# Kernel tuning notes

Hardware: AMD Instinct MI355X
Metric: run time of the kernel (lower is better)

Reference implementation:

```python
import jax, jax.numpy as jnp
import numpy as np

EMBED_DIM = 2048
NUM_HEADS = 16
HEAD_DIM = EMBED_DIM // NUM_HEADS  # 128
BLOCK_SIZE = 16
NUM_BLOCKS = 256  # max_seq_len 4096 / block_size 16
B = 64
T = 1  # single decode token per sequence (loop indexes k[i, 0, 0])


def setup_inputs() -> dict:
    key = jax.random.key(0)
    ks = jax.random.split(key, 12)
    w = 0.02
    return {
        "x": jax.random.normal(ks[0], (B, T, EMBED_DIM), jnp.float32),
        "k_cache": jax.random.normal(ks[1], (B, NUM_BLOCKS, BLOCK_SIZE, HEAD_DIM), jnp.float32),
        "v_cache": jax.random.normal(ks[2], (B, NUM_BLOCKS, BLOCK_SIZE, HEAD_DIM), jnp.float32),
        "cache_positions": jax.random.randint(ks[3], (B,), 0, NUM_BLOCKS * BLOCK_SIZE, jnp.int32),
        "Wq": jax.random.normal(ks[4], (EMBED_DIM, EMBED_DIM), jnp.float32) * w,
        "bq": jax.random.normal(ks[5], (EMBED_DIM,), jnp.float32) * w,
        "Wk": jax.random.normal(ks[6], (EMBED_DIM, HEAD_DIM), jnp.float32) * w,
        "bk": jax.random.normal(ks[7], (HEAD_DIM,), jnp.float32) * w,
        "Wv": jax.random.normal(ks[8], (EMBED_DIM, HEAD_DIM), jnp.float32) * w,
        "bv": jax.random.normal(ks[9], (HEAD_DIM,), jnp.float32) * w,
        "Wo": jax.random.normal(ks[10], (EMBED_DIM, EMBED_DIM), jnp.float32) * w,
        "bo": jax.random.normal(ks[11], (EMBED_DIM,), jnp.float32) * w,
    }


def reference(x, k_cache, v_cache, cache_positions, Wq, bq, Wk, bk, Wv, bv, Wo, bo):
    b, t, c = x.shape  # t == 1 (decode)
    hd = Wk.shape[1]
    h = c // hd
    scale = 1.0 / jnp.sqrt(jnp.asarray(hd, x.dtype))

    q = (x @ Wq + bq).reshape(b, t, h, hd)          # [B,1,H,hd]
    k_new = (x @ Wk + bk)[:, 0, :]                  # [B,hd] single KV head
    v_new = (x @ Wv + bv)[:, 0, :]                  # [B,hd]

    # Paged scatter: flatten (num_blocks, block_size) -> S slots; write new token at pos.
    s = k_cache.shape[1] * k_cache.shape[2]
    bidx = jnp.arange(b)
    kc = k_cache.reshape(b, s, hd).at[bidx, cache_positions].set(k_new)  # [B,S,hd]
    vc = v_cache.reshape(b, s, hd).at[bidx, cache_positions].set(v_new)

    # MQA: single KV head broadcast across H query heads. NOTE: softmax over the
    # FULL flattened cache (no validity mask), matching the original module.
    scores = jnp.einsum("bthd,bsd->bhts", q, kc) * scale   # [B,H,1,S]
    attn = jax.nn.softmax(scores, axis=-1)
    out = jnp.einsum("bhts,bsd->bthd", attn, vc).reshape(b, t, c)
    return out @ Wo + bo
```

## Files before the change

kernel.cpp:

```cpp
#include <hip/hip_runtime.h>
#include <math.h>

#define EMBED   2048
#define NHEADS  16
#define HD      128
#define S_TOT   4096
#define BATCH   64

typedef __attribute__((ext_vector_type(8))) short short8v;
typedef __attribute__((ext_vector_type(4))) short short4v;
typedef __attribute__((ext_vector_type(2))) short short2v;
typedef __attribute__((ext_vector_type(4))) float floatx4;

__device__ __forceinline__ unsigned short f2bf(float f) {
    unsigned u = __builtin_bit_cast(unsigned, f);
    u += 0x7fffu + ((u >> 16) & 1u);
    return (unsigned short)(u >> 16);
}

template <int CTRL>
__device__ __forceinline__ float dppf(float x) {
    int r = __builtin_amdgcn_mov_dpp(__builtin_bit_cast(int, x), CTRL, 0xF, 0xF, false);
    return __builtin_bit_cast(float, r);
}
__device__ __forceinline__ float rowmax16(float v) {
    v = fmaxf(v, dppf<0x121>(v));
    v = fmaxf(v, dppf<0x122>(v));
    v = fmaxf(v, dppf<0x124>(v));
    v = fmaxf(v, dppf<0x128>(v));
    return v;
}
__device__ __forceinline__ float rowsum16(float v) {
    v += dppf<0x121>(v);
    v += dppf<0x122>(v);
    v += dppf<0x124>(v);
    v += dppf<0x128>(v);
    return v;
}

__launch_bounds__(256)
__global__ void k1_qkv(const float* __restrict__ x,
                       const float* __restrict__ Wq, const float* __restrict__ bq,
                       const float* __restrict__ Wk, const float* __restrict__ bk,
                       const float* __restrict__ Wv, const float* __restrict__ bv,
                       float* __restrict__ qbuf, float* __restrict__ knew,
                       float* __restrict__ vnew) {
    const int tx = threadIdx.x & 31;
    const int ty = threadIdx.x >> 5;
    const int nt = blockIdx.x;
    const int kc = blockIdx.y;
    const int k0 = kc * 256;
    const int col0 = nt * 32;

    const float* W; const float* bias; float* out; int ldW;
    int cbase;
    if (col0 < 2048)       { W = Wq; bias = bq; out = qbuf; ldW = 2048; cbase = col0; }
    else if (col0 < 2176)  { W = Wk; bias = bk; out = knew; ldW = 128;  cbase = col0 - 2048; }
    else                   { W = Wv; bias = bv; out = vnew; ldW = 128;  cbase = col0 - 2176; }
    const int col = cbase + tx;

    __shared__ __align__(16) float xs[64][68];

    float acc[8] = {0, 0, 0, 0, 0, 0, 0, 0};

    for (int sub = 0; sub < 4; ++sub) {
        const int kb = k0 + sub * 64;
        #pragma unroll
        for (int i = 0; i < 4; ++i) {
            int c = threadIdx.x + i * 256;
            int r = c >> 4;
            int cc = (c & 15) << 2;
            float4 v = *(const float4*)(x + (size_t)r * EMBED + kb + cc);
            *(float4*)&xs[r][cc] = v;
        }
        __syncthreads();
        #pragma unroll
        for (int kk = 0; kk < 64; kk += 4) {
            float w0 = W[(size_t)(kb + kk + 0) * ldW + col];
            float w1 = W[(size_t)(kb + kk + 1) * ldW + col];
            float w2 = W[(size_t)(kb + kk + 2) * ldW + col];
            float w3 = W[(size_t)(kb + kk + 3) * ldW + col];
            #pragma unroll
            for (int j = 0; j < 8; ++j) {
                int m = ty + (j << 3);
                float4 xv = *(const float4*)&xs[m][kk];
                acc[j] = fmaf(xv.x, w0, acc[j]);
                acc[j] = fmaf(xv.y, w1, acc[j]);
                acc[j] = fmaf(xv.z, w2, acc[j]);
                acc[j] = fmaf(xv.w, w3, acc[j]);
            }
        }
        __syncthreads();
    }
    if (kc == 0) {
        float b = bias[col];
        #pragma unroll
        for (int j = 0; j < 8; ++j) acc[j] += b;
    }
    const int ldO = (ldW == 2048) ? 2048 : 128;
    #pragma unroll
    for (int j = 0; j < 8; ++j)
        atomicAdd(&out[(size_t)(ty + (j << 3)) * ldO + col], acc[j]);
}

__launch_bounds__(256)
__global__ void k2_attn(const float* __restrict__ qbuf,
                        const float* __restrict__ kcache,
                        const float* __restrict__ vcache,
                        const float* __restrict__ knew,
                        const float* __restrict__ vnew,
                        const int* __restrict__ cpos,
                        float* __restrict__ part_o,
                        float* __restrict__ part_ml)
{
    const int b = blockIdx.y;
    const int chunk = blockIdx.x;
    const int tid = threadIdx.x;
    const int w = tid >> 6;
    const int lane = tid & 63;
    const int quad = lane >> 4;
    const int lm = lane & 15;
    const int pos = cpos[b];

    __shared__ __align__(16) short qs[16 * 136];
    __shared__ __align__(16) short ksh[4][16 * 136];
    __shared__ __align__(16) short vsh[4][64 * 40];
    __shared__ __align__(16) short psh[4][16 * 40];

    {
        const int h = tid >> 4, d0 = (tid & 15) << 3;
        const float* src = qbuf + (size_t)b * EMBED + h * HD + d0;
        float4 a = *(const float4*)src;
        float4 c = *(const float4*)(src + 4);
        const float s = 0.08838834764831845f;
        short8v pk;
        pk[0] = f2bf(a.x * s); pk[1] = f2bf(a.y * s);
        pk[2] = f2bf(a.z * s); pk[3] = f2bf(a.w * s);
        pk[4] = f2bf(c.x * s); pk[5] = f2bf(c.y * s);
        pk[6] = f2bf(c.z * s); pk[7] = f2bf(c.w * s);
        *(short8v*)&qs[h * 136 + d0] = pk;
    }
    __syncthreads();

    short8v aq[4];
    #pragma unroll
    for (int t = 0; t < 4; ++t)
        aq[t] = *(short8v*)&qs[lm * 136 + t * 32 + quad * 8];

    short* kt = ksh[w];
    short* vt = vsh[w];
    short* pt = psh[w];

    float m_run[4] = {-INFINITY, -INFINITY, -INFINITY, -INFINITY};
    float l_run[4] = {0, 0, 0, 0};
    floatx4 oacc[8];
    #pragma unroll
    for (int i = 0; i < 8; ++i) oacc[i] = (floatx4){0, 0, 0, 0};

    const int sbase = chunk * 512 + w * 128;

    for (int st = 0; st < 4; ++st) {
        const int st0 = sbase + st * 32;
        floatx4 sc2[2];
        #pragma unroll
        for (int half = 0; half < 2; ++half) {
            const int s0 = st0 + half * 16;
            float4 tmp[8];
            #pragma unroll
            for (int i = 0; i < 8; ++i) {
                int f = i * 64 + lane;
                tmp[i] = *(const float4*)(kcache +
                    ((size_t)b * S_TOT + s0 + (f >> 5)) * HD + (f & 31) * 4);
            }
            #pragma unroll
            for (int i = 0; i < 8; ++i) {
                int f = i * 64 + lane;
                short4v pk;
                pk[0] = f2bf(tmp[i].x); pk[1] = f2bf(tmp[i].y);
                pk[2] = f2bf(tmp[i].z); pk[3] = f2bf(tmp[i].w);
                *(short4v*)&kt[(f >> 5) * 136 + (f & 31) * 4] = pk;
            }
            const int pr = pos - s0;
            if (pr >= 0 && pr < 16) {
                float2 kv = *(const float2*)(knew + b * HD + lane * 2);
                short2v p2; p2[0] = f2bf(kv.x); p2[1] = f2bf(kv.y);
                *(short2v*)&kt[pr * 136 + lane * 2] = p2;
            }
            floatx4 s = {0, 0, 0, 0};
            #pragma unroll
            for (int t = 0; t < 4; ++t) {
                short8v bk_ = *(short8v*)&kt[lm * 136 + t * 32 + quad * 8];
                s = __builtin_amdgcn_mfma_f32_16x16x32_bf16(aq[t], bk_, s, 0, 0, 0);
            }
            sc2[half] = s;
        }
        float alpha[4];
        #pragma unroll
        for (int r = 0; r < 4; ++r) {
            float mt = rowmax16(fmaxf(sc2[0][r], sc2[1][r]));
            float mn = fmaxf(m_run[r], mt);
            alpha[r] = __expf(m_run[r] - mn);
            m_run[r] = mn;
            float pA = __expf(sc2[0][r] - mn);
            float pB = __expf(sc2[1][r] - mn);
            float ss = rowsum16(pA + pB);
            l_run[r] = l_run[r] * alpha[r] + ss;
            pt[(quad * 4 + r) * 40 + lm]      = (short)f2bf(pA);
            pt[(quad * 4 + r) * 40 + 16 + lm] = (short)f2bf(pB);
        }
        #pragma unroll
        for (int dt = 0; dt < 8; ++dt) {
            oacc[dt][0] *= alpha[0]; oacc[dt][1] *= alpha[1];
            oacc[dt][2] *= alpha[2]; oacc[dt][3] *= alpha[3];
        }
        short8v ap = *(short8v*)&pt[lm * 40 + quad * 8];

        #pragma unroll
        for (int p = 0; p < 2; ++p) {
            const int sg = lane & 7;
            const int dgv = lane >> 3;
            #pragma unroll
            for (int i = 0; i < 2; ++i) {
                int dl = dgv * 4 + i * 32;
                int dglob = p * 64 + dl;
                const float* vb = vcache + ((size_t)b * S_TOT + st0 + sg * 4) * HD + dglob;
                float4 r0 = *(const float4*)(vb + 0 * HD);
                float4 r1 = *(const float4*)(vb + 1 * HD);
                float4 r2 = *(const float4*)(vb + 2 * HD);
                float4 r3 = *(const float4*)(vb + 3 * HD);
                short4v p0, p1, p2, p3;
                p0[0]=f2bf(r0.x); p0[1]=f2bf(r1.x); p0[2]=f2bf(r2.x); p0[3]=f2bf(r3.x);
                p1[0]=f2bf(r0.y); p1[1]=f2bf(r1.y); p1[2]=f2bf(r2.y); p1[3]=f2bf(r3.y);
                p2[0]=f2bf(r0.z); p2[1]=f2bf(r1.z); p2[2]=f2bf(r2.z); p2[3]=f2bf(r3.z);
                p3[0]=f2bf(r0.w); p3[1]=f2bf(r1.w); p3[2]=f2bf(r2.w); p3[3]=f2bf(r3.w);
                *(short4v*)&vt[(dl + 0) * 40 + sg * 4] = p0;
                *(short4v*)&vt[(dl + 1) * 40 + sg * 4] = p1;
                *(short4v*)&vt[(dl + 2) * 40 + sg * 4] = p2;
                *(short4v*)&vt[(dl + 3) * 40 + sg * 4] = p3;
            }
            const int prs = pos - st0;
            if (prs >= 0 && prs < 32) {
                float vvn = vnew[b * HD + p * 64 + lane];
                vt[lane * 40 + prs] = (short)f2bf(vvn);
            }
            #pragma unroll
            for (int dq = 0; dq < 4; ++dq) {
                int dt = p * 4 + dq;
                short8v bv_ = *(short8v*)&vt[(dq * 16 + lm) * 40 + quad * 8];
                oacc[dt] = __builtin_amdgcn_mfma_f32_16x16x32_bf16(ap, bv_, oacc[dt], 0, 0, 0);
            }
        }
    }

    const int cw = chunk * 4 + w;
    float* po = part_o + (size_t)(b * 32 + cw) * 16 * 128;
    #pragma unroll
    for (int dt = 0; dt < 8; ++dt)
        #pragma unroll
        for (int r = 0; r < 4; ++r)
            po[(quad * 4 + r) * 128 + dt * 16 + lm] = oacc[dt][r];
    if (lm < 2) {
        #pragma unroll
        for (int r = 0; r < 4; ++r) {
            float v = (lm == 0) ? m_run[r] : l_run[r];
            part_ml[((size_t)(b * 32 + cw) * 16 + quad * 4 + r) * 2 + lm] = v;
        }
    }
}

__launch_bounds__(128)
__global__ void k3_combine(const float* __restrict__ part_o,
                           const float* __restrict__ part_ml,
                           float* __restrict__ attn) {
    const int h = blockIdx.x, b = blockIdx.y, d = threadIdx.x;
    __shared__ float sm[32], sl[32];
    if (threadIdx.x < 32) {
        sm[threadIdx.x] = part_ml[((size_t)(b * 32 + threadIdx.x) * 16 + h) * 2 + 0];
        sl[threadIdx.x] = part_ml[((size_t)(b * 32 + threadIdx.x) * 16 + h) * 2 + 1];
    }
    __syncthreads();
    float M = -INFINITY;
    #pragma unroll
    for (int c = 0; c < 32; ++c) M = fmaxf(M, sm[c]);
    float O = 0.f, L = 0.f;
    for (int c = 0; c < 32; ++c) {
        float co = __expf(sm[c] - M);
        L += co * sl[c];
        O += co * part_o[((size_t)(b * 32 + c) * 16 + h) * 128 + d];
    }
    attn[(size_t)b * EMBED + h * HD + d] = O / L;
}

__launch_bounds__(256)
__global__ void k4_proj(const float* __restrict__ attn,
                        const float* __restrict__ Wo, const float* __restrict__ bo,
                        float* __restrict__ out) {
    const int tx = threadIdx.x & 31;
    const int ty = threadIdx.x >> 5;
    const int col = blockIdx.x * 32 + tx;
    const int k0 = blockIdx.y * 256;

    __shared__ __align__(16) float xs[64][68];
    float acc[8] = {0, 0, 0, 0, 0, 0, 0, 0};

    for (int sub = 0; sub < 4; ++sub) {
        const int kb = k0 + sub * 64;
        #pragma unroll
        for (int i = 0; i < 4; ++i) {
            int c = threadIdx.x + i * 256;
            int r = c >> 4;
            int cc = (c & 15) << 2;
            float4 v = *(const float4*)(attn + (size_t)r * EMBED + kb + cc);
            *(float4*)&xs[r][cc] = v;
        }
        __syncthreads();
        #pragma unroll
        for (int kk = 0; kk < 64; kk += 4) {
            float w0 = Wo[(size_t)(kb + kk + 0) * EMBED + col];
            float w1 = Wo[(size_t)(kb + kk + 1) * EMBED + col];
            float w2 = Wo[(size_t)(kb + kk + 2) * EMBED + col];
            float w3 = Wo[(size_t)(kb + kk + 3) * EMBED + col];
            #pragma unroll
            for (int j = 0; j < 8; ++j) {
                int m = ty + (j << 3);
                float4 xv = *(const float4*)&xs[m][kk];
                acc[j] = fmaf(xv.x, w0, acc[j]);
                acc[j] = fmaf(xv.y, w1, acc[j]);
                acc[j] = fmaf(xv.z, w2, acc[j]);
                acc[j] = fmaf(xv.w, w3, acc[j]);
            }
        }
        __syncthreads();
    }
    if (blockIdx.y == 0) {
        float b = bo[col];
        #pragma unroll
        for (int j = 0; j < 8; ++j) acc[j] += b;
    }
    #pragma unroll
    for (int j = 0; j < 8; ++j)
        atomicAdd(&out[(size_t)(ty + (j << 3)) * EMBED + col], acc[j]);
}

extern "C" void kernel_launch(void* const* d_in, const int* in_sizes, int n_in,
                              void* d_out, int out_size, void* d_ws, size_t ws_size,
                              hipStream_t stream) {
    (void)in_sizes; (void)n_in; (void)out_size; (void)ws_size;
    const float* x  = (const float*)d_in[0];
    const float* kc = (const float*)d_in[1];
    const float* vc = (const float*)d_in[2];
    const int*   cp = (const int*)d_in[3];
    const float* Wq = (const float*)d_in[4];
    const float* bq = (const float*)d_in[5];
    const float* Wk = (const float*)d_in[6];
    const float* bk = (const float*)d_in[7];
    const float* Wv = (const float*)d_in[8];
    const float* bv = (const float*)d_in[9];
    const float* Wo = (const float*)d_in[10];
    const float* bo = (const float*)d_in[11];
    float* out = (float*)d_out;
    float* ws  = (float*)d_ws;

    float* qbuf = ws;
    float* knew = ws + 131072;
    float* vnew = ws + 139264;
    float* attn = ws + 147456;
    float* po   = ws + 278528;
    float* pml  = ws + 4472832;

    hipMemsetAsync(qbuf, 0, 147456 * sizeof(float), stream);
    hipMemsetAsync(out, 0, (size_t)BATCH * EMBED * sizeof(float), stream);

    k1_qkv<<<dim3(72, 8), 256, 0, stream>>>(x, Wq, bq, Wk, bk, Wv, bv, qbuf, knew, vnew);
    k2_attn<<<dim3(8, 64), 256, 0, stream>>>(qbuf, kc, vc, knew, vnew, cp, po, pml);
    k3_combine<<<dim3(16, 64), 128, 0, stream>>>(po, pml, attn);
    k4_proj<<<dim3(64, 8), 256, 0, stream>>>(attn, Wo, bo, out);
}
```

Measured before the change: 395.2 us.

## Load K directly into MFMA registers and double attention split count

```diff
diff --git a/kernel.cpp b/kernel.cpp
--- a/kernel.cpp
+++ b/kernel.cpp
@@ -115,6 +115,10 @@
 {
     const int b = blockIdx.y;
     const int chunk = blockIdx.x;
+    const int nch = gridDim.x;
+    const int C = nch * 4;
+    const int spw = S_TOT / C;
+    const int nst = spw >> 5;
     const int tid = threadIdx.x;
     const int w = tid >> 6;
     const int lane = tid & 63;
@@ -123,7 +127,6 @@
     const int pos = cpos[b];
 
     __shared__ __align__(16) short qs[16 * 136];
-    __shared__ __align__(16) short ksh[4][16 * 136];
     __shared__ __align__(16) short vsh[4][64 * 40];
     __shared__ __align__(16) short psh[4][16 * 40];
 
@@ -147,7 +150,6 @@
     for (int t = 0; t < 4; ++t)
         aq[t] = *(short8v*)&qs[lm * 136 + t * 32 + quad * 8];
 
-    short* kt = ksh[w];
     short* vt = vsh[w];
     short* pt = psh[w];
 
@@ -157,39 +159,26 @@
     #pragma unroll
     for (int i = 0; i < 8; ++i) oacc[i] = (floatx4){0, 0, 0, 0};
 
-    const int sbase = chunk * 512 + w * 128;
-
-    for (int st = 0; st < 4; ++st) {
+    const int sbase = chunk * (S_TOT / nch) + w * spw;
+
+    for (int st = 0; st < nst; ++st) {
         const int st0 = sbase + st * 32;
         floatx4 sc2[2];
         #pragma unroll
         for (int half = 0; half < 2; ++half) {
             const int s0 = st0 + half * 16;
-            float4 tmp[8];
-            #pragma unroll
-            for (int i = 0; i < 8; ++i) {
-                int f = i * 64 + lane;
-                tmp[i] = *(const float4*)(kcache +
-                    ((size_t)b * S_TOT + s0 + (f >> 5)) * HD + (f & 31) * 4);
-            }
-            #pragma unroll
-            for (int i = 0; i < 8; ++i) {
-                int f = i * 64 + lane;
-                short4v pk;
-                pk[0] = f2bf(tmp[i].x); pk[1] = f2bf(tmp[i].y);
-                pk[2] = f2bf(tmp[i].z); pk[3] = f2bf(tmp[i].w);
-                *(short4v*)&kt[(f >> 5) * 136 + (f & 31) * 4] = pk;
-            }
-            const int pr = pos - s0;
-            if (pr >= 0 && pr < 16) {
-                float2 kv = *(const float2*)(knew + b * HD + lane * 2);
-                short2v p2; p2[0] = f2bf(kv.x); p2[1] = f2bf(kv.y);
-                *(short2v*)&kt[pr * 136 + lane * 2] = p2;
-            }
+            const float* krow = kcache + ((size_t)b * S_TOT + s0 + lm) * HD;
+            if (lm == pos - s0) krow = knew + (size_t)b * HD;
             floatx4 s = {0, 0, 0, 0};
             #pragma unroll
             for (int t = 0; t < 4; ++t) {
-                short8v bk_ = *(short8v*)&kt[lm * 136 + t * 32 + quad * 8];
+                float4 ka  = *(const float4*)(krow + t * 32 + quad * 8);
+                float4 kb2 = *(const float4*)(krow + t * 32 + quad * 8 + 4);
+                short8v bk_;
+                bk_[0] = f2bf(ka.x);  bk_[1] = f2bf(ka.y);
+                bk_[2] = f2bf(ka.z);  bk_[3] = f2bf(ka.w);
+                bk_[4] = f2bf(kb2.x); bk_[5] = f2bf(kb2.y);
+                bk_[6] = f2bf(kb2.z); bk_[7] = f2bf(kb2.w);
                 s = __builtin_amdgcn_mfma_f32_16x16x32_bf16(aq[t], bk_, s, 0, 0, 0);
             }
             sc2[half] = s;
@@ -253,7 +242,7 @@
     }
 
     const int cw = chunk * 4 + w;
-    float* po = part_o + (size_t)(b * 32 + cw) * 16 * 128;
+    float* po = part_o + (size_t)(b * C + cw) * 16 * 128;
     #pragma unroll
     for (int dt = 0; dt < 8; ++dt)
         #pragma unroll
@@ -263,7 +252,7 @@
         #pragma unroll
         for (int r = 0; r < 4; ++r) {
             float v = (lm == 0) ? m_run[r] : l_run[r];
-            part_ml[((size_t)(b * 32 + cw) * 16 + quad * 4 + r) * 2 + lm] = v;
+            part_ml[((size_t)(b * C + cw) * 16 + quad * 4 + r) * 2 + lm] = v;
         }
     }
 }
@@ -271,22 +260,21 @@
 __launch_bounds__(128)
 __global__ void k3_combine(const float* __restrict__ part_o,
                            const float* __restrict__ part_ml,
-                           float* __restrict__ attn) {
+                           float* __restrict__ attn, int C) {
     const int h = blockIdx.x, b = blockIdx.y, d = threadIdx.x;
-    __shared__ float sm[32], sl[32];
-    if (threadIdx.x < 32) {
-        sm[threadIdx.x] = part_ml[((size_t)(b * 32 + threadIdx.x) * 16 + h) * 2 + 0];
-        sl[threadIdx.x] = part_ml[((size_t)(b * 32 + threadIdx.x) * 16 + h) * 2 + 1];
+    __shared__ float sm[64], sl[64];
+    if (threadIdx.x < C) {
+        sm[threadIdx.x] = part_ml[((size_t)(b * C + threadIdx.x) * 16 + h) * 2 + 0];
+        sl[threadIdx.x] = part_ml[((size_t)(b * C + threadIdx.x) * 16 + h) * 2 + 1];
     }
     __syncthreads();
     float M = -INFINITY;
-    #pragma unroll
-    for (int c = 0; c < 32; ++c) M = fmaxf(M, sm[c]);
+    for (int c = 0; c < C; ++c) M = fmaxf(M, sm[c]);
     float O = 0.f, L = 0.f;
-    for (int c = 0; c < 32; ++c) {
+    for (int c = 0; c < C; ++c) {
         float co = __expf(sm[c] - M);
         L += co * sl[c];
-        O += co * part_o[((size_t)(b * 32 + c) * 16 + h) * 128 + d];
+        O += co * part_o[((size_t)(b * C + c) * 16 + h) * 128 + d];
     }
     attn[(size_t)b * EMBED + h * HD + d] = O / L;
 }
@@ -345,7 +333,7 @@
 extern "C" void kernel_launch(void* const* d_in, const int* in_sizes, int n_in,
                               void* d_out, int out_size, void* d_ws, size_t ws_size,
                               hipStream_t stream) {
-    (void)in_sizes; (void)n_in; (void)out_size; (void)ws_size;
+    (void)in_sizes; (void)n_in; (void)out_size;
     const float* x  = (const float*)d_in[0];
     const float* kc = (const float*)d_in[1];
     const float* vc = (const float*)d_in[2];
@@ -366,13 +354,17 @@
     float* vnew = ws + 139264;
     float* attn = ws + 147456;
     float* po   = ws + 278528;
-    float* pml  = ws + 4472832;
+
+    const size_t need16 = (278528ull + 64ull * 64 * 16 * 128 + 64ull * 64 * 16 * 2) * 4ull;
+    const int nch = (ws_size >= need16) ? 16 : 8;
+    const int C = nch * 4;
+    float* pml = po + (size_t)BATCH * C * 16 * 128;
 
     hipMemsetAsync(qbuf, 0, 147456 * sizeof(float), stream);
     hipMemsetAsync(out, 0, (size_t)BATCH * EMBED * sizeof(float), stream);
 
     k1_qkv<<<dim3(72, 8), 256, 0, stream>>>(x, Wq, bq, Wk, bk, Wv, bv, qbuf, knew, vnew);
-    k2_attn<<<dim3(8, 64), 256, 0, stream>>>(qbuf, kc, vc, knew, vnew, cp, po, pml);
-    k3_combine<<<dim3(16, 64), 128, 0, stream>>>(po, pml, attn);
+    k2_attn<<<dim3(nch, 64), 256, 0, stream>>>(qbuf, kc, vc, knew, vnew, cp, po, pml);
+    k3_combine<<<dim3(16, 64), 128, 0, stream>>>(po, pml, attn, C);
     k4_proj<<<dim3(64, 8), 256, 0, stream>>>(attn, Wo, bo, out);
 }
```

Measured after the change: 398.7 us. No clear change (+0.9%).
